# Kernel optimization log

Hardware: AMD Instinct MI355X
Metric: run time of the kernel (lower is better)

## Reference

```python
import jax, jax.numpy as jnp
import numpy as np

B, T, H, A, E, V = 32, 128, 1024, 1024, 512, 512  # A==H required by the module's cat/Linear shapes


def setup_inputs() -> dict:
    key = jax.random.key(0)
    ks = jax.random.split(key, 13)
    s = 0.02
    return {
        "encoder_outputs": jax.random.normal(ks[0], (B, A, E), jnp.float32),
        "hidden": jax.random.normal(ks[1], (1, B, H), jnp.float32),
        "target_seq": jax.random.normal(ks[2], (B, T, H), jnp.float32),
        "W_att": jax.random.normal(ks[3], (H + A, A), jnp.float32) * s,
        "b_att": jax.random.normal(ks[4], (A,), jnp.float32) * s,
        "W_comb": jax.random.normal(ks[5], (H + E, H), jnp.float32) * s,
        "b_comb": jax.random.normal(ks[6], (H,), jnp.float32) * s,
        "W_ih": jax.random.normal(ks[7], (3 * H, H), jnp.float32) * s,
        "b_ih": jax.random.normal(ks[8], (3 * H,), jnp.float32) * s,
        "W_hh": jax.random.normal(ks[9], (3 * H, H), jnp.float32) * s,
        "b_hh": jax.random.normal(ks[10], (3 * H,), jnp.float32) * s,
        "W_out": jax.random.normal(ks[11], (H, V), jnp.float32) * s,
        "b_out": jax.random.normal(ks[12], (V,), jnp.float32) * s,
    }


def reference(encoder_outputs, hidden, target_seq, W_att, b_att, W_comb, b_comb,
              W_ih, b_ih, W_hh, b_hh, W_out, b_out):
    # Teacher forcing: decoder input at step t is zeros (t=0) then target_seq[:, t-1]
    dec_in = jnp.concatenate([jnp.zeros_like(target_seq[:, :1]), target_seq[:, :-1]], axis=1)  # [B,T,H]
    dec_ts = jnp.swapaxes(dec_in, 0, 1)  # [T,B,H]

    def step(h, dec):  # h: [B,H], dec: [B,H]
        # attention over encoder positions (softmax width A == encoder seq len)
        attn = jax.nn.softmax(jnp.concatenate([dec, h], axis=1) @ W_att + b_att, axis=1)  # [B,A]
        ctx = jnp.einsum('bl,ble->be', attn, encoder_outputs)  # [B,E]
        g = jax.nn.relu(jnp.concatenate([dec, ctx], axis=1) @ W_comb + b_comb)  # [B,H]
        # GRU cell (torch gate order r, z, n)
        gi = g @ W_ih.T + b_ih
        gh = h @ W_hh.T + b_hh
        ir, iz, i_n = jnp.split(gi, 3, axis=1)
        hr, hz, h_n = jnp.split(gh, 3, axis=1)
        r = jax.nn.sigmoid(ir + hr)
        z = jax.nn.sigmoid(iz + hz)
        n = jnp.tanh(i_n + r * h_n)
        h_new = (1.0 - z) * n + z * h
        out_tok = h_new @ W_out + b_out  # [B,V]
        return h_new, out_tok

    h_last, outs = jax.lax.scan(step, hidden[0], dec_ts)  # outs: [T,B,V]
    output_seq = jnp.swapaxes(outs, 0, 1)  # [B,T,V]
    return output_seq, h_last[None]
```

## Files before the change

### kernel.cpp

```cpp
#include <hip/hip_runtime.h>

typedef unsigned short u16;
typedef unsigned int u32;
typedef unsigned long long u64;
typedef short v8s __attribute__((ext_vector_type(8)));
typedef float v4f __attribute__((ext_vector_type(4)));
typedef int v4i __attribute__((ext_vector_type(4)));

#define MFMA16(a, b, c) __builtin_amdgcn_mfma_f32_16x16x32_bf16((a), (b), (c), 0, 0, 0)

#define B_ 32
#define T_ 128
#define H_ 1024
#define A_ 1024
#define E_ 512
#define V_ 512
#define NBLK 256
#define NTH 512
#define NSLOT 32
#define ENC_LDS_BYTES 131072
#define SCRATCH_BYTES 28672
#define DSMEM_BYTES (ENC_LDS_BYTES + SCRATCH_BYTES)

__device__ __forceinline__ float b2f(u16 u) {
  union { u32 u; float f; } c; c.u = ((u32)u) << 16; return c.f;
}
__device__ __forceinline__ u16 f2b(float f) {
  union { float f; u32 u; } c; c.f = f;
  u32 x = c.u;
  x += 0x7fffu + ((x >> 16) & 1u);
  return (u16)(x >> 16);
}

__device__ __forceinline__ void ato_st(u32* p, u32 v) {
  __hip_atomic_store(p, v, __ATOMIC_RELAXED, __HIP_MEMORY_SCOPE_AGENT);
}
__device__ __forceinline__ void ato_stf(float* p, float v) {
  union { float f; u32 u; } c; c.f = v; ato_st((u32*)p, c.u);
}
__device__ __forceinline__ void ato_addf(float* p, float v) {
  __hip_atomic_fetch_add(p, v, __ATOMIC_RELAXED, __HIP_MEMORY_SCOPE_AGENT);
}

__device__ __forceinline__ v4i ld16_sc1(const void* p) {
  v4i r;
  asm volatile("global_load_dwordx4 %0, %1, off sc1" : "=v"(r) : "v"(p));
  return r;
}
__device__ __forceinline__ float ld4_sc1(const void* p) {
  float r;
  asm volatile("global_load_dword %0, %1, off sc1" : "=v"(r) : "v"(p));
  return r;
}
__device__ __forceinline__ void wait_vm0() {
  asm volatile("s_waitcnt vmcnt(0)" ::: "memory");
  __builtin_amdgcn_sched_barrier(0);
}
__device__ __forceinline__ v8s as8(v4i x) { union { v4i a; v8s b; } u; u.a = x; return u.b; }
__device__ __forceinline__ void cvt8(v4i qa, v4i qb, v8s& hi, v8s& lo) {
  union { v4i q; float f[4]; } a, b;
  a.q = qa; b.q = qb;
  float v[8] = {a.f[0], a.f[1], a.f[2], a.f[3], b.f[0], b.f[1], b.f[2], b.f[3]};
  u16 hh[8], ll[8];
  #pragma unroll
  for (int i = 0; i < 8; ++i) {
    float x = fmaxf(v[i], 0.f);
    u16 hv = f2b(x);
    hh[i] = hv; ll[i] = f2b(x - b2f(hv));
  }
  hi = *(v8s*)hh; lo = *(v8s*)ll;
}

__device__ __forceinline__ void post_sem(u32* slots, int idx, u32 ep) {
  asm volatile("s_waitcnt vmcnt(0)" ::: "memory");
  __syncthreads();
  if (threadIdx.x == 0)
    __hip_atomic_store(slots + idx * NSLOT, ep, __ATOMIC_RELAXED, __HIP_MEMORY_SCOPE_AGENT);
}
__device__ __forceinline__ void wait_sem(const u32* slots, int n, u32 ep) {
  if (threadIdx.x < (unsigned)n) {
    while (__hip_atomic_load(slots + threadIdx.x * NSLOT, __ATOMIC_RELAXED, __HIP_MEMORY_SCOPE_AGENT) < ep)
      __builtin_amdgcn_s_sleep(8);
  }
  __syncthreads();
  asm volatile("" ::: "memory");
}

__device__ __forceinline__ void gemm_nk(const u16* ah, const u16* al, size_t mstr,
                                        const u16* bp, int nk, v4f& c0, v4f& c1) {
  #pragma unroll 2
  for (int i = 0; i < nk; ++i) {
    v8s b   = *(const v8s*)(bp);
    v8s a0h = *(const v8s*)(ah);
    v8s a1h = *(const v8s*)(ah + mstr);
    v8s a0l = *(const v8s*)(al);
    v8s a1l = *(const v8s*)(al + mstr);
    c0 = MFMA16(a0h, b, c0);
    c1 = MFMA16(a1h, b, c1);
    c0 = MFMA16(a0l, b, c0);
    c1 = MFMA16(a1l, b, c1);
    ah += 32; al += 32; bp += 32;
  }
}

__device__ __forceinline__ void red_store2(float* part, int wv, int lane, v4f c0, v4f c1) {
  float* p = part + (wv * 64 + lane) * 8;
  #pragma unroll
  for (int r = 0; r < 4; ++r) { p[r] = c0[r]; p[4 + r] = c1[r]; }
}
__device__ __forceinline__ float red_sum2(const float* part, int o) {
  int m = o >> 4, n = o & 15;
  int lane = (((m & 15) >> 2) << 4) + n;
  int idx = ((m >> 4) << 2) + (m & 3);
  float s = 0.f;
  #pragma unroll
  for (int w = 0; w < 8; ++w) s += part[(w * 64 + lane) * 8 + idx];
  return s;
}

__global__ void __launch_bounds__(NTH, 1)
dec_persist(const u16* __restrict__ tgt_hi, const u16* __restrict__ tgt_lo,
            const u16* __restrict__ WattT, const u16* __restrict__ Whh_b,
            const u16* __restrict__ Wih_b, const u16* __restrict__ WcombT,
            const u16* __restrict__ Wc_ctxT,
            const float* __restrict__ enc_f,
            const float* __restrict__ batt, const float* __restrict__ bcomb,
            const float* __restrict__ bih, const float* __restrict__ bhh,
            float* h, float* logit, float* gh, float* g_acc, float* logit_dec,
            u16* hbf_hi, u16* hbf_lo, u16* hseqb, u32* sems)
{
  const int tid = threadIdx.x;
  const int bid = blockIdx.x;
  const int lane = tid & 63;
  const int wv = tid >> 6;
  const int ln = lane & 15;
  const int kq8 = (lane >> 4) * 8;

  u32* S1 = sems;
  u32* S2 = sems + 64 * NSLOT;
  u32* S3 = sems + (64 + 256) * NSLOT;

  extern __shared__ __align__(16) unsigned char dsm[];
  u16* lds_enc = (u16*)dsm;
  float* scratch = (float*)(dsm + ENC_LDS_BYTES);

  {
    int b = bid >> 3, e0 = (bid & 7) * 64;
    const float* src = enc_f + (size_t)b * A_ * E_ + e0 + (tid & 7) * 8;
    int seg = (tid & 7) * 8;
    for (int i = 0; i < 16; ++i) {
      int row = i * 64 + (tid >> 3);
      const float* sp = src + (size_t)row * E_;
      float4 a = *(const float4*)sp;
      float4 bq = *(const float4*)(sp + 4);
      u16 tmp[8] = {f2b(a.x), f2b(a.y), f2b(a.z), f2b(a.w),
                    f2b(bq.x), f2b(bq.y), f2b(bq.z), f2b(bq.w)};
      *(v8s*)(lds_enc + row * 64 + seg) = *(v8s*)tmp;
    }
  }

  for (int t = 0; t < T_; ++t) {
    u32 ep = (u32)(t + 1);
    {
      float* part = scratch;
      size_t a0 = (size_t)ln * H_ + wv * 128 + kq8;
      v4i ah0[4], ah1[4], al0[4], al1[4];
      #pragma unroll
      for (int i = 0; i < 4; ++i) {
        ah0[i] = ld16_sc1(hbf_hi + a0 + i * 32);
        ah1[i] = ld16_sc1(hbf_hi + a0 + 16 * H_ + i * 32);
        al0[i] = ld16_sc1(hbf_lo + a0 + i * 32);
        al1[i] = ld16_sc1(hbf_lo + a0 + 16 * H_ + i * 32);
      }
      float ldec = 0.f;
      const u16* bp;
      int n0;
      if (bid < 64) {
        int gi = bid * 512 + tid;
        ato_stf(&g_acc[((t + 1) & 1) * (B_ * H_) + gi], bcomb[gi & (H_ - 1)]);
        n0 = bid * 16;
        ldec = ld4_sc1(&logit_dec[(t & 1) * (B_ * A_) + (tid >> 4) * A_ + n0 + (tid & 15)]);
        bp = WattT + (size_t)(n0 + ln) * 2048 + 1024 + wv * 128 + kq8;
      } else {
        n0 = (bid - 64) * 16;
        bp = Whh_b + (size_t)(n0 + ln) * H_ + wv * 128 + kq8;
      }
      v8s wb[4];
      #pragma unroll
      for (int i = 0; i < 4; ++i) wb[i] = *(const v8s*)(bp + i * 32);
      v4f c0 = {0.f, 0.f, 0.f, 0.f}, c1 = {0.f, 0.f, 0.f, 0.f};
      wait_vm0();
      #pragma unroll
      for (int i = 0; i < 4; ++i) {
        c0 = MFMA16(as8(ah0[i]), wb[i], c0);
        c1 = MFMA16(as8(ah1[i]), wb[i], c1);
        c0 = MFMA16(as8(al0[i]), wb[i], c0);
        c1 = MFMA16(as8(al1[i]), wb[i], c1);
      }
      red_store2(part, wv, lane, c0, c1);
      __syncthreads();
      {
        float s = red_sum2(part, tid);
        int m = tid >> 4, n = tid & 15;
        if (bid < 64) {
          ato_stf(&logit[m * A_ + n0 + n], s + ldec);
        } else {
          ato_stf(&gh[(size_t)(n0 + n) * 32 + m], s + bhh[n0 + n]);
        }
      }
    }
    if (bid < 64) post_sem(S1, bid, ep);
    wait_sem(S1, 64, ep);

    {
      float* p    = scratch;
      float* part = scratch + 1024;
      float* red  = scratch + 5120;
      float* sctx = scratch + 5136;
      int b = bid >> 3, es = bid & 7;
      float v1 = ld4_sc1(&logit[b * A_ + tid]);
      float v2 = ld4_sc1(&logit[b * A_ + 512 + tid]);
      wait_vm0();
      float mx = fmaxf(v1, v2);
      #pragma unroll
      for (int off = 32; off; off >>= 1) mx = fmaxf(mx, __shfl_xor(mx, off));
      if (lane == 0) red[wv] = mx;
      __syncthreads();
      float mfull = red[0];
      #pragma unroll
      for (int q = 1; q < 8; ++q) mfull = fmaxf(mfull, red[q]);
      float e1 = __expf(v1 - mfull), e2 = __expf(v2 - mfull);
      p[tid] = e1; p[512 + tid] = e2;
      float sm = e1 + e2;
      #pragma unroll
      for (int off = 32; off; off >>= 1) sm += __shfl_xor(sm, off);
      if (lane == 0) red[8 + wv] = sm;
      __syncthreads();
      float ssum = red[8];
      #pragma unroll
      for (int q = 1; q < 8; ++q) ssum += red[8 + q];
      float inv = 1.f / ssum;

      int le = lane & 7, lr = lane >> 3;
      float acc[8] = {0.f, 0.f, 0.f, 0.f, 0.f, 0.f, 0.f, 0.f};
      #pragma unroll 4
      for (int i = 0; i < 16; ++i) {
        int l = i * 64 + wv * 8 + lr;
        v8s w = *(const v8s*)(lds_enc + l * 64 + le * 8);
        float pv = p[l];
        #pragma unroll
        for (int r = 0; r < 8; ++r) acc[r] += pv * b2f((u16)w[r]);
      }
      float* pp = part + ((wv * 8 + lr) * 8 + le) * 8;
      #pragma unroll
      for (int r = 0; r < 8; ++r) pp[r] = acc[r];
      __syncthreads();
      if (tid < 64) {
        int eo = tid >> 3, r = tid & 7;
        float s = 0.f;
        #pragma unroll
        for (int q = 0; q < 64; ++q) s += part[q * 64 + eo * 8 + r];
        sctx[tid] = s * inv;
      }
      __syncthreads();
      {
        const u16* w0 = Wc_ctxT + (size_t)(2 * tid) * E_ + es * 64;
        const u16* w1 = w0 + E_;
        float a0 = 0.f, a1 = 0.f;
        #pragma unroll
        for (int i = 0; i < 8; ++i) {
          v8s q0 = *(const v8s*)(w0 + i * 8);
          v8s q1 = *(const v8s*)(w1 + i * 8);
          #pragma unroll
          for (int r = 0; r < 8; ++r) {
            float pv = sctx[i * 8 + r];
            a0 += pv * b2f((u16)q0[r]);
            a1 += pv * b2f((u16)q1[r]);
          }
        }
        float* gp = g_acc + (t & 1) * (B_ * H_) + b * H_ + 2 * tid;
        ato_addf(gp, a0);
        ato_addf(gp + 1, a1);
      }
    }
    post_sem(S2, bid, ep);
    if (bid < 64) wait_sem(S2, NBLK, ep);

    {
      if (bid < 64) {
        float* part = scratch;
        float* hx   = scratch + 6144;
        int j0 = bid * 16;
        const float* gbase = g_acc + (t & 1) * (B_ * H_);
        int koff0 = wv * 128 + kq8;
        v4i gr0[8], gr1[8];
        #pragma unroll
        for (int i = 0; i < 4; ++i) {
          const float* p0 = gbase + (size_t)ln * H_ + koff0 + i * 32;
          const float* p1 = gbase + (size_t)(ln + 16) * H_ + koff0 + i * 32;
          gr0[2 * i]     = ld16_sc1(p0);
          gr0[2 * i + 1] = ld16_sc1(p0 + 4);
          gr1[2 * i]     = ld16_sc1(p1);
          gr1[2 * i + 1] = ld16_sc1(p1 + 4);
        }
        const u16* bp0 = Wih_b + (size_t)(j0 + ln) * H_ + koff0;
        const u16* bp1 = bp0 + (size_t)H_ * H_;
        const u16* bp2 = bp0 + (size_t)2 * H_ * H_;
        v8s wb0[4], wb1[4], wb2[4];
        #pragma unroll
        for (int i = 0; i < 4; ++i) {
          wb0[i] = *(const v8s*)(bp0 + i * 32);
          wb1[i] = *(const v8s*)(bp1 + i * 32);
          wb2[i] = *(const v8s*)(bp2 + i * 32);
        }
        v4f c00 = {0.f,0.f,0.f,0.f}, c01 = c00, c02 = c00, c10 = c00, c11 = c00, c12 = c00;
        wait_vm0();
        #pragma unroll
        for (int i = 0; i < 4; ++i) {
          v8s a0h, a0l, a1h, a1l;
          cvt8(gr0[2 * i], gr0[2 * i + 1], a0h, a0l);
          cvt8(gr1[2 * i], gr1[2 * i + 1], a1h, a1l);
          c00 = MFMA16(a0h, wb0[i], c00); c00 = MFMA16(a0l, wb0[i], c00);
          c01 = MFMA16(a0h, wb1[i], c01); c01 = MFMA16(a0l, wb1[i], c01);
          c02 = MFMA16(a0h, wb2[i], c02); c02 = MFMA16(a0l, wb2[i], c02);
          c10 = MFMA16(a1h, wb0[i], c10); c10 = MFMA16(a1l, wb0[i], c10);
          c11 = MFMA16(a1h, wb1[i], c11); c11 = MFMA16(a1l, wb1[i], c11);
          c12 = MFMA16(a1h, wb2[i], c12); c12 = MFMA16(a1l, wb2[i], c12);
        }
        float hr0 = 0.f, hz0 = 0.f, hn0 = 0.f, hr1 = 0.f, hz1 = 0.f, hn1 = 0.f;
        float ho0 = 0.f, ho1 = 0.f;
        int obl = tid >> 4, jj = tid & 15, j = j0 + jj;
        if (tid < 256) {
          hr0 = ld4_sc1(&gh[(size_t)j * 32 + obl]);
          hz0 = ld4_sc1(&gh[(size_t)(H_ + j) * 32 + obl]);
          hn0 = ld4_sc1(&gh[(size_t)(2 * H_ + j) * 32 + obl]);
          hr1 = ld4_sc1(&gh[(size_t)j * 32 + 16 + obl]);
          hz1 = ld4_sc1(&gh[(size_t)(H_ + j) * 32 + 16 + obl]);
          hn1 = ld4_sc1(&gh[(size_t)(2 * H_ + j) * 32 + 16 + obl]);
          ho0 = h[obl * H_ + j];
          ho1 = h[(obl + 16) * H_ + j];
        }
        float bi_r = 0.f, bi_z = 0.f, bi_n = 0.f;
        if (tid < 256) {
          bi_r = bih[j]; bi_z = bih[H_ + j]; bi_n = bih[2 * H_ + j];
        }
        #pragma unroll
        for (int pass = 0; pass < 2; ++pass) {
          float* pp = part + (wv * 64 + lane) * 12;
          if (pass == 0) {
            #pragma unroll
            for (int r = 0; r < 4; ++r) { pp[r] = c00[r]; pp[4 + r] = c01[r]; pp[8 + r] = c02[r]; }
          } else {
            #pragma unroll
            for (int r = 0; r < 4; ++r) { pp[r] = c10[r]; pp[4 + r] = c11[r]; pp[8 + r] = c12[r]; }
          }
          __syncthreads();
          if (tid < 256) {
            if (pass == 0) wait_vm0();
            int ob = pass * 16 + obl;
            int lanei = ((obl >> 2) << 4) + jj;
            int rg = obl & 3;
            float ir = 0.f, iz = 0.f, in_ = 0.f;
            #pragma unroll
            for (int w = 0; w < 8; ++w) {
              const float* q = part + (w * 64 + lanei) * 12;
              ir += q[rg]; iz += q[4 + rg]; in_ += q[8 + rg];
            }
            ir += bi_r; iz += bi_z; in_ += bi_n;
            float hr = pass ? hr1 : hr0;
            float hz = pass ? hz1 : hz0;
            float hn = pass ? hn1 : hn0;
            float ho = pass ? ho1 : ho0;
            float r = 1.f / (1.f + __expf(-(ir + hr)));
            float z = 1.f / (1.f + __expf(-(iz + hz)));
            float n = tanhf(in_ + r * hn);
            float hnew = (1.f - z) * n + z * ho;
            h[ob * H_ + j] = hnew;
            hx[ob * 16 + jj] = hnew;
          }
          __syncthreads();
        }
        if (tid < 256) {
          int ob2 = tid >> 3, j2 = (tid & 7) * 2;
          float v0 = hx[ob2 * 16 + j2], v1 = hx[ob2 * 16 + j2 + 1];
          u16 h0 = f2b(v0), h1 = f2b(v1);
          u16 l0 = f2b(v0 - b2f(h0)), l1 = f2b(v1 - b2f(h1));
          int idx = ob2 * H_ + j0 + j2;
          u32 hp = (u32)h0 | ((u32)h1 << 16);
          ato_st((u32*)(hbf_hi + idx), hp);
          ato_st((u32*)(hbf_lo + idx), (u32)l0 | ((u32)l1 << 16));
          *(u32*)(hseqb + ((size_t)t * 32 + ob2) * H_ + j0 + j2) = hp;
        }
      } else if (bid < 128) {
        if (t < T_ - 1) {
          float* part = scratch;
          int n0 = (bid - 64) * 16;
          v4f c0 = {0.f, 0.f, 0.f, 0.f}, c1 = {0.f, 0.f, 0.f, 0.f};
          size_t abase = ((size_t)ln * T_ + t) * H_ + wv * 128 + kq8;
          const u16* bp = WattT + (size_t)(n0 + ln) * 2048 + wv * 128 + kq8;
          gemm_nk(tgt_hi + abase, tgt_lo + abase, (size_t)16 * T_ * H_, bp, 4, c0, c1);
          red_store2(part, wv, lane, c0, c1);
          __syncthreads();
          int m = tid >> 4, n = tid & 15;
          ato_stf(&logit_dec[((t + 1) & 1) * (B_ * A_) + m * A_ + n0 + n],
                  red_sum2(part, tid) + batt[n0 + n]);
        }
      } else if (bid < 192) {
        if (t < T_ - 1) {
          float* part = scratch;
          int n0 = (bid - 128) * 16;
          v4f c0 = {0.f, 0.f, 0.f, 0.f}, c1 = {0.f, 0.f, 0.f, 0.f};
          size_t abase = ((size_t)ln * T_ + t) * H_ + wv * 128 + kq8;
          const u16* bp = WcombT + (size_t)(n0 + ln) * 1536 + wv * 128 + kq8;
          gemm_nk(tgt_hi + abase, tgt_lo + abase, (size_t)16 * T_ * H_, bp, 4, c0, c1);
          red_store2(part, wv, lane, c0, c1);
          __syncthreads();
          int m = tid >> 4, n = tid & 15;
          ato_addf(&g_acc[((t + 1) & 1) * (B_ * H_) + m * H_ + n0 + n], red_sum2(part, tid));
        }
      }
    }
    if (bid < 192) post_sem(S3, bid, ep);
    wait_sem(S3, 192, ep);
  }
}

__global__ void __launch_bounds__(256, 2)
out_gemm(const u16* __restrict__ hseqb, const u16* __restrict__ WoutT,
         const float* __restrict__ bout, float* __restrict__ out)
{
  int tid = threadIdx.x, lane = tid & 63, wv = tid >> 6;
  int ln = lane & 15, kq8 = (lane >> 4) * 8;
  int m0 = (blockIdx.x >> 3) * 32;
  int n0 = (blockIdx.x & 7) * 64 + wv * 16;
  v4f c0 = {0.f, 0.f, 0.f, 0.f}, c1 = {0.f, 0.f, 0.f, 0.f};
  const u16* ap = hseqb + (size_t)(m0 + ln) * 1024 + kq8;
  const u16* bp = WoutT + (size_t)(n0 + ln) * 1024 + kq8;
  for (int i = 0; i < 32; ++i) {
    v8s b = *(const v8s*)bp;
    v8s a0 = *(const v8s*)ap;
    v8s a1 = *(const v8s*)(ap + 16 * 1024);
    c0 = MFMA16(a0, b, c0);
    c1 = MFMA16(a1, b, c1);
    ap += 32; bp += 32;
  }
  int v = n0 + ln;
  float bo = bout[v];
  int rbase = (lane >> 4) * 4;
  #pragma unroll
  for (int rg = 0; rg < 4; ++rg) {
    int m = m0 + rbase + rg;
    out[((size_t)(m & 31) * T_ + (m >> 5)) * V_ + v] = c0[rg] + bo;
    int m2 = m + 16;
    out[((size_t)(m2 & 31) * T_ + (m2 >> 5)) * V_ + v] = c1[rg] + bo;
  }
}

__global__ void __launch_bounds__(256)
hlast_copy(const float* __restrict__ h, float* __restrict__ out)
{
  int i = blockIdx.x * 256 + threadIdx.x;
  if (i < B_ * H_) out[(size_t)B_ * T_ * V_ + i] = h[i];
}

__global__ void __launch_bounds__(256)
k_cvt(const float* __restrict__ in, u16* __restrict__ out, int n)
{
  int stride = gridDim.x * 256;
  for (int i = blockIdx.x * 256 + threadIdx.x; i < n; i += stride) out[i] = f2b(in[i]);
}

__global__ void __launch_bounds__(256)
k_cvt_split(const float* __restrict__ in, u16* __restrict__ hi, u16* __restrict__ lo, int n)
{
  int stride = gridDim.x * 256;
  for (int i = blockIdx.x * 256 + threadIdx.x; i < n; i += stride) {
    float x = in[i];
    u16 a = f2b(x);
    hi[i] = a;
    lo[i] = f2b(x - b2f(a));
  }
}

__global__ void __launch_bounds__(256)
k_tr(const float* __restrict__ in, u16* __restrict__ out, int R, int C)
{
  __shared__ float tile[32][33];
  int tc = C >> 5;
  int r0 = (blockIdx.x / tc) << 5, c0 = (blockIdx.x % tc) << 5;
  int tx = threadIdx.x & 31, ty = threadIdx.x >> 5;
  #pragma unroll
  for (int q = 0; q < 4; ++q) {
    int r = ty + q * 8;
    tile[r][tx] = in[(size_t)(r0 + r) * C + c0 + tx];
  }
  __syncthreads();
  #pragma unroll
  for (int q = 0; q < 4; ++q) {
    int r = ty + q * 8;
    out[(size_t)(c0 + r) * R + r0 + tx] = f2b(tile[tx][r]);
  }
}

__global__ void __launch_bounds__(256)
k_init(const float* __restrict__ hidden, const float* __restrict__ bcomb,
       float* h, u16* hhi, u16* hlo, float* g_acc)
{
  int i = blockIdx.x * 256 + threadIdx.x;
  if (i < B_ * H_) {
    float x = hidden[i];
    h[i] = x;
    u16 a = f2b(x);
    hhi[i] = a;
    hlo[i] = f2b(x - b2f(a));
    g_acc[i] = bcomb[i & (H_ - 1)];
  }
}

extern "C" void kernel_launch(void* const* d_in, const int* in_sizes, int n_in,
                              void* d_out, int out_size, void* d_ws, size_t ws_size,
                              hipStream_t stream) {
  (void)in_sizes; (void)n_in; (void)out_size; (void)ws_size;
  const float* enc    = (const float*)d_in[0];
  const float* hidden = (const float*)d_in[1];
  const float* tgt    = (const float*)d_in[2];
  const float* Watt   = (const float*)d_in[3];
  const float* batt   = (const float*)d_in[4];
  const float* Wcomb  = (const float*)d_in[5];
  const float* bcomb  = (const float*)d_in[6];
  const float* Wih    = (const float*)d_in[7];
  const float* bih    = (const float*)d_in[8];
  const float* Whh    = (const float*)d_in[9];
  const float* bhh    = (const float*)d_in[10];
  const float* Wout   = (const float*)d_in[11];
  const float* bout   = (const float*)d_in[12];

  size_t off = 0;
  char* base = (char*)d_ws;
  auto alloc = [&](size_t bytes) -> void* {
    void* p = base + off;
    off += (bytes + 255) & ~(size_t)255;
    return p;
  };
  size_t sem_bytes = (size_t)(64 + 256 + 192) * NSLOT * 4;
  u32*   sems   = (u32*)  alloc(sem_bytes);
  float* h      = (float*)alloc(B_ * H_ * 4);
  float* logit  = (float*)alloc(B_ * A_ * 4);
  float* gh     = (float*)alloc((size_t)3 * H_ * B_ * 4);
  float* g_acc  = (float*)alloc((size_t)2 * B_ * H_ * 4);
  float* logit_dec = (float*)alloc((size_t)2 * B_ * A_ * 4);
  u16*   hbf_hi = (u16*)  alloc(B_ * H_ * 2);
  u16*   hbf_lo = (u16*)  alloc(B_ * H_ * 2);
  u16*   hseqb  = (u16*)  alloc((size_t)T_ * B_ * H_ * 2);
  u16*   tgt_hi = (u16*)  alloc((size_t)B_ * T_ * H_ * 2);
  u16*   tgt_lo = (u16*)  alloc((size_t)B_ * T_ * H_ * 2);
  u16*   WattT  = (u16*)  alloc((size_t)2048 * 1024 * 2);
  u16*   Whh_b  = (u16*)  alloc((size_t)3 * H_ * H_ * 2);
  u16*   Wih_b  = (u16*)  alloc((size_t)3 * H_ * H_ * 2);
  u16*   WcombT = (u16*)  alloc((size_t)1024 * 1536 * 2);
  u16*   Wc_ctxT= (u16*)  alloc((size_t)1024 * 512 * 2);
  u16*   WoutT  = (u16*)  alloc((size_t)512 * 1024 * 2);

  hipMemsetAsync(sems, 0, sem_bytes, stream);
  hipMemsetAsync(logit_dec, 0, (size_t)2 * B_ * A_ * 4, stream);

  k_cvt_split<<<2048, 256, 0, stream>>>(tgt, tgt_hi, tgt_lo, B_ * T_ * H_);
  k_cvt<<<2048, 256, 0, stream>>>(Whh, Whh_b, 3 * H_ * H_);
  k_cvt<<<2048, 256, 0, stream>>>(Wih, Wih_b, 3 * H_ * H_);
  k_tr<<<64 * 32, 256, 0, stream>>>(Watt, WattT, 2048, 1024);
  k_tr<<<48 * 32, 256, 0, stream>>>(Wcomb, WcombT, 1536, 1024);
  k_tr<<<16 * 32, 256, 0, stream>>>(Wcomb + (size_t)1024 * H_, Wc_ctxT, 512, 1024);
  k_tr<<<32 * 16, 256, 0, stream>>>(Wout, WoutT, 1024, 512);
  k_init<<<128, 256, 0, stream>>>(hidden, bcomb, h, hbf_hi, hbf_lo, g_acc);

  hipFuncSetAttribute((const void*)dec_persist,
                      hipFuncAttributeMaxDynamicSharedMemorySize, DSMEM_BYTES);

  dec_persist<<<NBLK, NTH, DSMEM_BYTES, stream>>>(tgt_hi, tgt_lo, WattT, Whh_b, Wih_b,
                                                  WcombT, Wc_ctxT, enc,
                                                  batt, bcomb, bih, bhh,
                                                  h, logit, gh, g_acc, logit_dec,
                                                  hbf_hi, hbf_lo, hseqb, sems);
  out_gemm<<<1024, 256, 0, stream>>>(hseqb, WoutT, bout, (float*)d_out);
  hlast_copy<<<128, 256, 0, stream>>>(h, (float*)d_out);
}
```

Baseline: 3.936 ms.

## Fuse output projection into persistent decoder and use uniform grid barriers

Removes the separate out_gemm launch and computes the per-step output projection for step t-1 inside the persistent kernel on four otherwise idle blocks during phase 1, with a final tail step after the loop. Phase 1 work is consolidated onto 128 blocks, each computing 32 columns instead of 16. The per-phase producer/consumer semaphores are replaced by a full all-block barrier with a shorter sleep. The full barriers force every block to wait at each phase instead of only the needed subsets, trading extra synchronization for removing the tail GEMM.

```diff
diff --git a/kernel.cpp b/kernel.cpp
--- a/kernel.cpp
+++ b/kernel.cpp
@@ -71,16 +71,14 @@
   hi = *(v8s*)hh; lo = *(v8s*)ll;
 }
 
-__device__ __forceinline__ void post_sem(u32* slots, int idx, u32 ep) {
+__device__ __forceinline__ void grid_bar(u32* arr, u32 ep) {
   asm volatile("s_waitcnt vmcnt(0)" ::: "memory");
   __syncthreads();
   if (threadIdx.x == 0)
-    __hip_atomic_store(slots + idx * NSLOT, ep, __ATOMIC_RELAXED, __HIP_MEMORY_SCOPE_AGENT);
-}
-__device__ __forceinline__ void wait_sem(const u32* slots, int n, u32 ep) {
-  if (threadIdx.x < (unsigned)n) {
-    while (__hip_atomic_load(slots + threadIdx.x * NSLOT, __ATOMIC_RELAXED, __HIP_MEMORY_SCOPE_AGENT) < ep)
-      __builtin_amdgcn_s_sleep(8);
+    __hip_atomic_store(arr + blockIdx.x * NSLOT, ep, __ATOMIC_RELAXED, __HIP_MEMORY_SCOPE_AGENT);
+  if (threadIdx.x < NBLK) {
+    while (__hip_atomic_load(arr + threadIdx.x * NSLOT, __ATOMIC_RELAXED, __HIP_MEMORY_SCOPE_AGENT) < ep)
+      __builtin_amdgcn_s_sleep(1);
   }
   __syncthreads();
   asm volatile("" ::: "memory");
@@ -122,12 +120,13 @@
 dec_persist(const u16* __restrict__ tgt_hi, const u16* __restrict__ tgt_lo,
             const u16* __restrict__ WattT, const u16* __restrict__ Whh_b,
             const u16* __restrict__ Wih_b, const u16* __restrict__ WcombT,
-            const u16* __restrict__ Wc_ctxT,
+            const u16* __restrict__ Wc_ctxT, const u16* __restrict__ WoutT,
             const float* __restrict__ enc_f,
             const float* __restrict__ batt, const float* __restrict__ bcomb,
             const float* __restrict__ bih, const float* __restrict__ bhh,
+            const float* __restrict__ bout,
             float* h, float* logit, float* gh, float* g_acc, float* logit_dec,
-            u16* hbf_hi, u16* hbf_lo, u16* hseqb, u32* sems)
+            u16* hbf_hi, u16* hbf_lo, u16* hseqb, float* outp, u32* bar)
 {
   const int tid = threadIdx.x;
   const int bid = blockIdx.x;
@@ -135,10 +134,6 @@
   const int wv = tid >> 6;
   const int ln = lane & 15;
   const int kq8 = (lane >> 4) * 8;
-
-  u32* S1 = sems;
-  u32* S2 = sems + 64 * NSLOT;
-  u32* S3 = sems + (64 + 256) * NSLOT;
 
   extern __shared__ __align__(16) unsigned char dsm[];
   u16* lds_enc = (u16*)dsm;
@@ -159,9 +154,10 @@
     }
   }
 
+  u32 ep = 0;
+
   for (int t = 0; t < T_; ++t) {
-    u32 ep = (u32)(t + 1);
-    {
+    if (bid < 128) {
       float* part = scratch;
       size_t a0 = (size_t)ln * H_ + wv * 128 + kq8;
       v4i ah0[4], ah1[4], al0[4], al1[4];
@@ -172,45 +168,85 @@
         al0[i] = ld16_sc1(hbf_lo + a0 + i * 32);
         al1[i] = ld16_sc1(hbf_lo + a0 + 16 * H_ + i * 32);
       }
-      float ldec = 0.f;
-      const u16* bp;
+      const u16* bpA;
+      size_t bstride;
+      float ldec0 = 0.f, ldec1 = 0.f;
       int n0;
-      if (bid < 64) {
-        int gi = bid * 512 + tid;
+      if (bid < 32) {
+        int gi = bid * 1024 + tid;
         ato_stf(&g_acc[((t + 1) & 1) * (B_ * H_) + gi], bcomb[gi & (H_ - 1)]);
-        n0 = bid * 16;
-        ldec = ld4_sc1(&logit_dec[(t & 1) * (B_ * A_) + (tid >> 4) * A_ + n0 + (tid & 15)]);
-        bp = WattT + (size_t)(n0 + ln) * 2048 + 1024 + wv * 128 + kq8;
+        ato_stf(&g_acc[((t + 1) & 1) * (B_ * H_) + gi + 512], bcomb[(gi + 512) & (H_ - 1)]);
+        n0 = bid * 32;
+        const float* lp = logit_dec + (size_t)(t & 1) * (B_ * A_) + (tid >> 4) * A_ + n0 + (tid & 15);
+        ldec0 = ld4_sc1(lp);
+        ldec1 = ld4_sc1(lp + 16);
+        bpA = WattT + (size_t)(n0 + ln) * 2048 + 1024 + wv * 128 + kq8;
+        bstride = 2048;
       } else {
-        n0 = (bid - 64) * 16;
-        bp = Whh_b + (size_t)(n0 + ln) * H_ + wv * 128 + kq8;
-      }
-      v8s wb[4];
-      #pragma unroll
-      for (int i = 0; i < 4; ++i) wb[i] = *(const v8s*)(bp + i * 32);
-      v4f c0 = {0.f, 0.f, 0.f, 0.f}, c1 = {0.f, 0.f, 0.f, 0.f};
+        n0 = (bid - 32) * 32;
+        bpA = Whh_b + (size_t)(n0 + ln) * H_ + wv * 128 + kq8;
+        bstride = H_;
+      }
+      const u16* bpB = bpA + 16 * bstride;
+      v8s wA[4], wB[4];
+      #pragma unroll
+      for (int i = 0; i < 4; ++i) {
+        wA[i] = *(const v8s*)(bpA + i * 32);
+        wB[i] = *(const v8s*)(bpB + i * 32);
+      }
+      v4f cA0 = {0.f,0.f,0.f,0.f}, cA1 = cA0, cB0 = cA0, cB1 = cA0;
       wait_vm0();
       #pragma unroll
       for (int i = 0; i < 4; ++i) {
-        c0 = MFMA16(as8(ah0[i]), wb[i], c0);
-        c1 = MFMA16(as8(ah1[i]), wb[i], c1);
-        c0 = MFMA16(as8(al0[i]), wb[i], c0);
-        c1 = MFMA16(as8(al1[i]), wb[i], c1);
-      }
-      red_store2(part, wv, lane, c0, c1);
+        v8s h0 = as8(ah0[i]), h1 = as8(ah1[i]);
+        v8s l0 = as8(al0[i]), l1 = as8(al1[i]);
+        cA0 = MFMA16(h0, wA[i], cA0); cA1 = MFMA16(h1, wA[i], cA1);
+        cA0 = MFMA16(l0, wA[i], cA0); cA1 = MFMA16(l1, wA[i], cA1);
+        cB0 = MFMA16(h0, wB[i], cB0); cB1 = MFMA16(h1, wB[i], cB1);
+        cB0 = MFMA16(l0, wB[i], cB0); cB1 = MFMA16(l1, wB[i], cB1);
+      }
+      red_store2(part, wv, lane, cA0, cA1);
       __syncthreads();
       {
         float s = red_sum2(part, tid);
         int m = tid >> 4, n = tid & 15;
-        if (bid < 64) {
-          ato_stf(&logit[m * A_ + n0 + n], s + ldec);
-        } else {
-          ato_stf(&gh[(size_t)(n0 + n) * 32 + m], s + bhh[n0 + n]);
+        if (bid < 32) ato_stf(&logit[m * A_ + n0 + n], s + ldec0);
+        else          ato_stf(&gh[(size_t)(n0 + n) * 32 + m], s + bhh[n0 + n]);
+      }
+      __syncthreads();
+      red_store2(part, wv, lane, cB0, cB1);
+      __syncthreads();
+      {
+        float s = red_sum2(part, tid);
+        int m = tid >> 4, n = tid & 15;
+        if (bid < 32) ato_stf(&logit[m * A_ + n0 + 16 + n], s + ldec1);
+        else          ato_stf(&gh[(size_t)(n0 + 16 + n) * 32 + m], s + bhh[n0 + 16 + n]);
+      }
+    } else if (bid < 132) {
+      if (t >= 1) {
+        int n0o = (bid - 128) * 128 + wv * 16;
+        const u16* ap = hseqb + ((size_t)(t - 1) * 32 + ln) * H_ + kq8;
+        const u16* bp = WoutT + (size_t)(n0o + ln) * 1024 + kq8;
+        v4f c0 = {0.f, 0.f, 0.f, 0.f}, c1 = {0.f, 0.f, 0.f, 0.f};
+        for (int i = 0; i < 32; ++i) {
+          v8s b = *(const v8s*)bp;
+          v8s a0 = *(const v8s*)ap;
+          v8s a1 = *(const v8s*)(ap + 16 * H_);
+          c0 = MFMA16(a0, b, c0);
+          c1 = MFMA16(a1, b, c1);
+          ap += 32; bp += 32;
+        }
+        int v = n0o + ln;
+        float bo = bout[v];
+        int rb = (lane >> 4) * 4;
+        #pragma unroll
+        for (int r = 0; r < 4; ++r) {
+          outp[((size_t)(rb + r) * T_ + (t - 1)) * V_ + v] = c0[r] + bo;
+          outp[((size_t)(rb + r + 16) * T_ + (t - 1)) * V_ + v] = c1[r] + bo;
         }
       }
     }
-    if (bid < 64) post_sem(S1, bid, ep);
-    wait_sem(S1, 64, ep);
+    grid_bar(bar, ++ep);
 
     {
       float* p    = scratch;
@@ -283,8 +319,7 @@
         ato_addf(gp + 1, a1);
       }
     }
-    post_sem(S2, bid, ep);
-    if (bid < 64) wait_sem(S2, NBLK, ep);
+    grid_bar(bar, ++ep);
 
     {
       if (bid < 64) {
@@ -389,7 +424,7 @@
           u32 hp = (u32)h0 | ((u32)h1 << 16);
           ato_st((u32*)(hbf_hi + idx), hp);
           ato_st((u32*)(hbf_lo + idx), (u32)l0 | ((u32)l1 << 16));
-          *(u32*)(hseqb + ((size_t)t * 32 + ob2) * H_ + j0 + j2) = hp;
+          ato_st((u32*)(hseqb + ((size_t)t * 32 + ob2) * H_ + j0 + j2), hp);
         }
       } else if (bid < 128) {
         if (t < T_ - 1) {
@@ -420,39 +455,32 @@
         }
       }
     }
-    if (bid < 192) post_sem(S3, bid, ep);
-    wait_sem(S3, 192, ep);
-  }
-}
-
-__global__ void __launch_bounds__(256, 2)
-out_gemm(const u16* __restrict__ hseqb, const u16* __restrict__ WoutT,
-         const float* __restrict__ bout, float* __restrict__ out)
-{
-  int tid = threadIdx.x, lane = tid & 63, wv = tid >> 6;
-  int ln = lane & 15, kq8 = (lane >> 4) * 8;
-  int m0 = (blockIdx.x >> 3) * 32;
-  int n0 = (blockIdx.x & 7) * 64 + wv * 16;
-  v4f c0 = {0.f, 0.f, 0.f, 0.f}, c1 = {0.f, 0.f, 0.f, 0.f};
-  const u16* ap = hseqb + (size_t)(m0 + ln) * 1024 + kq8;
-  const u16* bp = WoutT + (size_t)(n0 + ln) * 1024 + kq8;
-  for (int i = 0; i < 32; ++i) {
-    v8s b = *(const v8s*)bp;
-    v8s a0 = *(const v8s*)ap;
-    v8s a1 = *(const v8s*)(ap + 16 * 1024);
-    c0 = MFMA16(a0, b, c0);
-    c1 = MFMA16(a1, b, c1);
-    ap += 32; bp += 32;
-  }
-  int v = n0 + ln;
-  float bo = bout[v];
-  int rbase = (lane >> 4) * 4;
-  #pragma unroll
-  for (int rg = 0; rg < 4; ++rg) {
-    int m = m0 + rbase + rg;
-    out[((size_t)(m & 31) * T_ + (m >> 5)) * V_ + v] = c0[rg] + bo;
-    int m2 = m + 16;
-    out[((size_t)(m2 & 31) * T_ + (m2 >> 5)) * V_ + v] = c1[rg] + bo;
+    grid_bar(bar, ++ep);
+  }
+
+  grid_bar(bar, ++ep);
+  if (bid >= 128 && bid < 132) {
+    int t = T_;
+    int n0o = (bid - 128) * 128 + wv * 16;
+    const u16* ap = hseqb + ((size_t)(t - 1) * 32 + ln) * H_ + kq8;
+    const u16* bp = WoutT + (size_t)(n0o + ln) * 1024 + kq8;
+    v4f c0 = {0.f, 0.f, 0.f, 0.f}, c1 = {0.f, 0.f, 0.f, 0.f};
+    for (int i = 0; i < 32; ++i) {
+      v8s b = *(const v8s*)bp;
+      v8s a0 = *(const v8s*)ap;
+      v8s a1 = *(const v8s*)(ap + 16 * H_);
+      c0 = MFMA16(a0, b, c0);
+      c1 = MFMA16(a1, b, c1);
+      ap += 32; bp += 32;
+    }
+    int v = n0o + ln;
+    float bo = bout[v];
+    int rb = (lane >> 4) * 4;
+    #pragma unroll
+    for (int r = 0; r < 4; ++r) {
+      outp[((size_t)(rb + r) * T_ + (t - 1)) * V_ + v] = c0[r] + bo;
+      outp[((size_t)(rb + r + 16) * T_ + (t - 1)) * V_ + v] = c1[r] + bo;
+    }
   }
 }
 
@@ -542,8 +570,8 @@
     off += (bytes + 255) & ~(size_t)255;
     return p;
   };
-  size_t sem_bytes = (size_t)(64 + 256 + 192) * NSLOT * 4;
-  u32*   sems   = (u32*)  alloc(sem_bytes);
+  size_t bar_bytes = (size_t)(NBLK * NSLOT + 64) * 4;
+  u32*   bar    = (u32*)  alloc(bar_bytes);
   float* h      = (float*)alloc(B_ * H_ * 4);
   float* logit  = (float*)alloc(B_ * A_ * 4);
   float* gh     = (float*)alloc((size_t)3 * H_ * B_ * 4);
@@ -561,7 +589,7 @@
   u16*   Wc_ctxT= (u16*)  alloc((size_t)1024 * 512 * 2);
   u16*   WoutT  = (u16*)  alloc((size_t)512 * 1024 * 2);
 
-  hipMemsetAsync(sems, 0, sem_bytes, stream);
+  hipMemsetAsync(bar, 0, bar_bytes, stream);
   hipMemsetAsync(logit_dec, 0, (size_t)2 * B_ * A_ * 4, stream);
 
   k_cvt_split<<<2048, 256, 0, stream>>>(tgt, tgt_hi, tgt_lo, B_ * T_ * H_);
@@ -577,10 +605,9 @@
                       hipFuncAttributeMaxDynamicSharedMemorySize, DSMEM_BYTES);
 
   dec_persist<<<NBLK, NTH, DSMEM_BYTES, stream>>>(tgt_hi, tgt_lo, WattT, Whh_b, Wih_b,
-                                                  WcombT, Wc_ctxT, enc,
-                                                  batt, bcomb, bih, bhh,
+                                                  WcombT, Wc_ctxT, WoutT, enc,
+                                                  batt, bcomb, bih, bhh, bout,
                                                   h, logit, gh, g_acc, logit_dec,
-                                                  hbf_hi, hbf_lo, hseqb, sems);
-  out_gemm<<<1024, 256, 0, stream>>>(hseqb, WoutT, bout, (float*)d_out);
+                                                  hbf_hi, hbf_lo, hseqb, (float*)d_out, bar);
   hlast_copy<<<128, 256, 0, stream>>>(h, (float*)d_out);
 }
```

Measured after the change: 6.009 ms. +52.7%, slower.
